# Performance work log

Hardware: AMD Instinct MI355X
Metric: run time of the kernel (lower is better)

## Reference

```python
import jax, jax.numpy as jnp
import numpy as np

B, N, E = 8, 4096, 65536
H, DH, GH = 4, 16, 64            # gat heads, head_dim, gat hidden
EDGE_EMBED = 16
D_FUSION = 640 + 64 + 640 + 40   # 1384


def setup_inputs() -> dict:
    key = jax.random.key(0)
    ks = jax.random.split(key, 24)
    rn = lambda i, shape, s=0.05: jax.random.normal(ks[i], shape, dtype=jnp.float32) * s
    return {
        'rnafm': rn(0, (B, 640), 1.0),
        'edit_delta': rn(1, (B, 640), 1.0),
        'hand_feat': rn(2, (B, 40), 1.0),
        'node_feats': rn(3, (B, N, 22), 1.0),
        'edge_index': jax.random.randint(ks[4], (B, 2, E), 0, N, dtype=jnp.int32),
        'edge_type': jax.random.randint(ks[5], (B, E), 0, 3, dtype=jnp.int32),
        'node_proj_w': rn(6, (GH, 22)), 'node_proj_b': jnp.zeros((GH,), jnp.float32),
        'gat_W': rn(7, (3, GH, GH)),
        'gat_a_src': rn(8, (3, H, DH)), 'gat_a_dst': rn(9, (3, H, DH)),
        'gat_a_edge': rn(10, (3, H, EDGE_EMBED)),
        'gat_edge_embed': rn(11, (3, 3, EDGE_EMBED)),
        'gat_ln_g': jnp.ones((3, GH), jnp.float32), 'gat_ln_b': jnp.zeros((3, GH), jnp.float32),
        'gat_out_w': rn(12, (64, GH)), 'gat_out_b': jnp.zeros((64,), jnp.float32),
        'enc1_w': rn(13, (256, D_FUSION)), 'enc1_b': jnp.zeros((256,), jnp.float32),
        'enc_ln_g': jnp.ones((256,), jnp.float32), 'enc_ln_b': jnp.zeros((256,), jnp.float32),
        'enc2_w': rn(14, (128, 256)), 'enc2_b': jnp.zeros((128,), jnp.float32),
        'bin_w': rn(15, (1, 128)), 'bin_b': jnp.zeros((1,), jnp.float32),
        'adp1_w': rn(16, (5, 32, 128)), 'adp1_b': jnp.zeros((5, 32), jnp.float32),
        'adp2_w': rn(17, (5, 1, 32)), 'adp2_b': jnp.zeros((5, 1), jnp.float32),
        'cls1_w': rn(18, (64, 128)), 'cls1_b': jnp.zeros((64,), jnp.float32),
        'cls2_w': rn(19, (6, 64)), 'cls2_b': jnp.zeros((6,), jnp.float32),
    }


def _layernorm(x, g, b, eps=1e-5):
    m = x.mean(-1, keepdims=True)
    v = ((x - m) ** 2).mean(-1, keepdims=True)
    return (x - m) / jnp.sqrt(v + eps) * g + b


def _gat_layer(x, src, dst, et, W, a_src, a_dst, a_edge, eemb, g, b):
    """x: [N, GH] -> [N, GH]; per-edge attention + scatter-softmax + scatter-add."""
    n = x.shape[0]
    h = x @ W.T                          # [N, GH]
    hh = h.reshape(n, H, DH)
    h_src, h_dst = hh[src], hh[dst]      # [E, H, DH] gathers
    attn = (jnp.einsum('ehd,hd->eh', h_src, a_src)
            + jnp.einsum('ehd,hd->eh', h_dst, a_dst)
            + eemb[et] @ a_edge.T)       # [E, H]
    attn = jnp.where(attn >= 0, attn, 0.2 * attn)  # leaky_relu(0.2)
    amax = jnp.maximum(jax.ops.segment_max(attn, dst, num_segments=n), -1e9)
    ex = jnp.exp(attn - amax[dst])
    denom = jax.ops.segment_sum(ex, dst, num_segments=n)
    an = ex / (denom[dst] + 1e-10)       # dropout is identity in eval
    agg = jax.ops.segment_sum(h_src * an[:, :, None], dst, num_segments=n)
    return _layernorm(agg.reshape(n, H * DH) + h, g, b)


def reference(rnafm, edit_delta, hand_feat, node_feats, edge_index, edge_type,
              node_proj_w, node_proj_b, gat_W, gat_a_src, gat_a_dst, gat_a_edge,
              gat_edge_embed, gat_ln_g, gat_ln_b, gat_out_w, gat_out_b,
              enc1_w, enc1_b, enc_ln_g, enc_ln_b, enc2_w, enc2_b,
              bin_w, bin_b, adp1_w, adp1_b, adp2_w, adp2_b,
              cls1_w, cls1_b, cls2_w, cls2_b):
    gelu = lambda t: jax.nn.gelu(t, approximate=False)

    def per_graph(nf, ei, et):
        x = nf @ node_proj_w.T + node_proj_b
        for l in range(3):
            x = gelu(_gat_layer(x, ei[0], ei[1], et, gat_W[l], gat_a_src[l],
                                gat_a_dst[l], gat_a_edge[l], gat_edge_embed[l],
                                gat_ln_g[l], gat_ln_b[l]))
        return x[x.shape[0] // 2]        # center node embedding

    gat_emb = jax.vmap(per_graph)(node_feats, edge_index, edge_type)   # [B, GH]
    gat_o = gat_emb @ gat_out_w.T + gat_out_b                          # [B, 64]
    fused = jnp.concatenate([rnafm, gat_o, edit_delta, hand_feat], axis=-1)
    h1 = _layernorm(gelu(fused @ enc1_w.T + enc1_b), enc_ln_g, enc_ln_b)
    shared = gelu(h1 @ enc2_w.T + enc2_b)                              # [B, 128]
    binary = (shared @ bin_w.T + bin_b)[:, 0]                          # [B]
    a1 = gelu(jnp.einsum('bf,hif->bhi', shared, adp1_w) + adp1_b)      # [B, 5, 32]
    per_enz = jnp.einsum('bhi,hi->bh', a1, adp2_w[:, 0, :]) + adp2_b[:, 0]  # [B, 5]
    cls = gelu(shared @ cls1_w.T + cls1_b) @ cls2_w.T + cls2_b         # [B, 6]
    return (binary, per_enz, cls, shared)
```

## Files before the change

### kernel.cpp

```cpp
#include <hip/hip_runtime.h>
#include <hip/hip_bf16.h>
#include <math.h>

#define BB 8
#define NN 4096
#define EE 65536
#define LOG2E 1.4426950408889634f

__device__ __forceinline__ float my_erf(float x){
  float ax = fabsf(x);
  float tt = 1.f/(1.f + 0.3275911f*ax);
  float poly = ((((1.061405429f*tt - 1.453152027f)*tt + 1.421413741f)*tt
                 - 0.284496736f)*tt + 0.254829592f)*tt;
  float y = 1.f - poly*expf(-ax*ax);
  return x >= 0.f ? y : -y;
}
__device__ __forceinline__ float gelu_f(float x){ return 0.5f*x*(1.0f + my_erf(x*0.7071067811865476f)); }
__device__ __forceinline__ float ld(const void* p, long i){ return ((const float*)p)[i]; }

__global__ __launch_bounds__(256) void k_pre(
    const void* __restrict__ nf, const void* __restrict__ pw, const void* __restrict__ pb,
    const void* __restrict__ W, const void* __restrict__ a_src, const void* __restrict__ a_dst,
    const void* __restrict__ a_edge, const void* __restrict__ eemb,
    const int* __restrict__ ei, const int* __restrict__ ety,
    float* __restrict__ h, float* __restrict__ sdot, float* __restrict__ ebt,
    int* __restrict__ cursor, int* __restrict__ csr, int b0, int nb, int NF){
  if ((int)blockIdx.x < NF){
    int fi = (int)blockIdx.x;
    int bpb = NF / nb;
    int b, q;
    if (nb == BB){ b = fi & 7; q = fi >> 3; }
    else         { b = fi / bpb; q = fi - b*bpb; }
    int e4 = q*256 + threadIdx.x;
    const int* base = ei + (long)(b0+b)*2*EE;
    int4 s4 = ((const int4*)base)[e4];
    int4 d4 = ((const int4*)(base + EE))[e4];
    int4 t4 = ((const int4*)(ety + (long)(b0+b)*EE))[e4];
    int* cb = cursor + b*NN;
    int ss[4] = {s4.x & (NN-1), s4.y & (NN-1), s4.z & (NN-1), s4.w & (NN-1)};
    int dd[4] = {d4.x & (NN-1), d4.y & (NN-1), d4.z & (NN-1), d4.w & (NN-1)};
    int tt[4] = {t4.x, t4.y, t4.z, t4.w};
    #pragma unroll
    for (int i=0;i<4;i++){
      int ty = tt[i]; ty = (ty < 0) ? 0 : (ty > 2 ? 2 : ty);
      int p = atomicAdd(&cb[dd[i]], 1);
      if (p < 64) csr[((long)(b*NN) + dd[i])*64 + p] = ss[i] | (ty << 12);
    }
    return;
  }

  __attribute__((aligned(16))) __shared__ float wlT[64*68];
  __attribute__((aligned(16))) __shared__ float nfl[32*24];
  __attribute__((aligned(16))) __shared__ float xs[32*68];
  int t = threadIdx.x;
  int lb = (int)blockIdx.x - NF;

  if (lb == 0 && t < 48){
    int ll = t >> 4, r = t & 15;
    if (r < 12){
      int ty = r >> 2, hd2 = r & 3;
      float s = 0.f;
      #pragma unroll
      for (int k=0;k<16;k++)
        s += ld(eemb, ll*48 + ty*16 + k) * ld(a_edge, ll*64 + hd2*16 + k);
      ebt[t] = s * LOG2E;
    }
  }
  {
    #pragma unroll
    for (int idx = t; idx < 1024; idx += 256){
      int row = idx >> 4, chunk = idx & 15;
      float4 wv = *((const float4*)((const float*)W + row*64 + chunk*4));
      *((float4*)&wlT[row*68 + chunk*4]) = wv;
    }
  }
  {
    long nfbase = ((long)b0*NN + (long)lb*32)*22;
    for (int idx = t; idx < 704; idx += 256){
      int row = idx / 22, k = idx - row*22;
      nfl[row*24 + k] = ld(nf, nfbase + idx);
    }
  }

  int w = t >> 6;
  int c = t & 63;
  int hd = c >> 4, dd = c & 15;
  long n0 = (long)lb*32 + w*8;

  float wreg[22];
  #pragma unroll
  for (int k = 0; k < 22; k++) wreg[k] = ld(pw, c*22 + k);
  float bias = ld(pb, c);
  __syncthreads();
  if (n0 >= nb*NN) return;

  #pragma unroll
  for (int i=0;i<8;i++){
    const float* nr = nfl + (w*8+i)*24;
    float a = bias;
    #pragma unroll
    for (int kc = 0; kc < 5; kc++){
      float4 nv = *((const float4*)&nr[kc*4]);
      a += nv.x*wreg[kc*4] + nv.y*wreg[kc*4+1] + nv.z*wreg[kc*4+2] + nv.w*wreg[kc*4+3];
    }
    a += nr[20]*wreg[20] + nr[21]*wreg[21];
    xs[(w*8+i)*68 + c] = a;
  }

  float acc[8] = {0.f,0.f,0.f,0.f,0.f,0.f,0.f,0.f};
  const float* xw = xs + (w*8)*68;
  const float* wr2 = wlT + c*68;
  #pragma unroll 4
  for (int kk=0;kk<16;kk++){
    float4 wv = *((const float4*)&wr2[kk*4]);
    #pragma unroll
    for (int i=0;i<8;i++){
      float4 xv = *((const float4*)&xw[i*68 + kk*4]);
      acc[i] += xv.x*wv.x + xv.y*wv.y + xv.z*wv.z + xv.w*wv.w;
    }
  }

  float cas = ld(a_src, c) * LOG2E;
  float cad = ld(a_dst, c) * LOG2E;
  #pragma unroll
  for (int i=0;i<8;i++){
    h[(n0+i)*64 + c] = acc[i];
    float ps = acc[i]*cas, pd = acc[i]*cad;
    #pragma unroll
    for (int o=8;o>=1;o>>=1){
      ps += __shfl_xor(ps,o,64);
      pd += __shfl_xor(pd,o,64);
    }
    if (dd == 0){
      sdot[(n0+i)*8 + hd]     = ps;
      sdot[(n0+i)*8 + 4 + hd] = pd;
    }
  }
}

__device__ __forceinline__ float gat_node(const float* __restrict__ hb,
    const float* __restrict__ sb, const int* __restrict__ cb, int dg,
    float sdP, float ebP0, float ebP1, float ebP2,
    float hdst, int c, int hd,
    const void* lng, const void* lnb, int l){
  int hL = c & 3;
  float denP = 0.f, acc = 0.f;
  int npass = (dg + 15) >> 4;
  for (int p = 0; p < npass; p++){
    int eidx = (p << 4) + (c >> 2);
    int pk = cb[eidx];
    int src = pk & 4095, ty = (pk >> 12) & 3;
    float av = sb[src*8 + hL] + sdP + (ty==0?ebP0:(ty==1?ebP1:ebP2));
    av = fmaxf(av, 0.2f*av);
    float ev = exp2f(av);
    if (eidx >= dg) ev = 0.f;
    denP += ev;
    int jmax = dg - (p << 4); if (jmax > 16) jmax = 16;
    #pragma unroll 4
    for (int j = 0; j < jmax; j++){
      float evj = __shfl(ev, j*4 + hd, 64);
      int sj = __builtin_amdgcn_readlane(pk, j*4) & 4095;
      acc += hb[(long)sj*64 + c] * evj;
    }
  }
  #pragma unroll
  for (int o=4;o<=32;o<<=1) denP += __shfl_xor(denP, o, 64);
  float den = __shfl(denP, hd, 64);
  float y = acc / (den + 1e-10f) + hdst;

  float s = y;
  #pragma unroll
  for (int o=32;o>=1;o>>=1) s += __shfl_xor(s, o, 64);
  float mean = s * (1.f/64.f);
  float d = y - mean;
  float vs = d*d;
  #pragma unroll
  for (int o=32;o>=1;o>>=1) vs += __shfl_xor(vs, o, 64);
  float var = vs * (1.f/64.f);
  float outv = d * rsqrtf(var + 1e-5f) * ld(lng, l*64+c) + ld(lnb, l*64+c);
  return gelu_f(outv);
}

__device__ __forceinline__ long swizzle_wave(int bi, int w, int nb){
  if (nb == BB) return (long)(bi & 7)*NN + (long)(bi >> 3)*4 + w;
  return (long)bi*4 + w;
}

__global__ __launch_bounds__(256) void k_gatlin(
    const float* __restrict__ hIn, const float* __restrict__ sdIn,
    const float* __restrict__ ebt,
    const int* __restrict__ cursor, const int* __restrict__ csr,
    const void* __restrict__ lng, const void* __restrict__ lnb,
    const void* __restrict__ W,
    const void* __restrict__ a_src, const void* __restrict__ a_dst,
    float* __restrict__ hOut, float* __restrict__ sdOut,
    int l, int nb){
  __attribute__((aligned(16))) __shared__ float wlT[64*68];
  __attribute__((aligned(16))) __shared__ float xs[4*68];
  int t = threadIdx.x;
  {
    #pragma unroll
    for (int idx = t; idx < 1024; idx += 256){
      int row = idx >> 4, chunk = idx & 15;
      float4 wv = *((const float4*)((const float*)W + (long)(l+1)*4096 + row*64 + chunk*4));
      *((float4*)&wlT[row*68 + chunk*4]) = wv;
    }
  }
  __syncthreads();

  int wloc = t >> 6;
  long wave = swizzle_wave(blockIdx.x, wloc, nb);
  if (wave >= nb*NN) return;
  int c  = t & 63;
  int hd = c >> 4, dd = c & 15, hL = c & 3;
  int b  = (int)(wave >> 12);

  float ebP0 = ebt[l*16 + 0 + hL];
  float ebP1 = ebt[l*16 + 4 + hL];
  float ebP2 = ebt[l*16 + 8 + hL];
  float sdP  = sdIn[wave*8 + 4 + hL];
  float hdst = hIn[wave*64 + c];
  int dg = __builtin_amdgcn_readfirstlane(cursor[wave]);
  dg = (dg < 0) ? 0 : (dg > 64 ? 64 : dg);
  const int* cb = csr + wave*64;
  const float* hb = hIn + (long)(b*NN)*64;
  const float* sb = sdIn + (long)(b*NN)*8;

  float g = gat_node(hb, sb, cb, dg, sdP, ebP0, ebP1, ebP2, hdst, c, hd, lng, lnb, l);

  xs[wloc*68 + c] = g;
  float ha = 0.f;
  const float* xw = xs + wloc*68;
  const float* wr = wlT + c*68;
  #pragma unroll 4
  for (int kk=0;kk<16;kk++){
    float4 xv = *((const float4*)&xw[kk*4]);
    float4 wv = *((const float4*)&wr[kk*4]);
    ha += xv.x*wv.x + xv.y*wv.y + xv.z*wv.z + xv.w*wv.w;
  }
  hOut[wave*64 + c] = ha;
  float cas = ld(a_src, (long)(l+1)*64 + c) * LOG2E;
  float cad = ld(a_dst, (long)(l+1)*64 + c) * LOG2E;
  float ps = ha*cas, pd = ha*cad;
  #pragma unroll
  for (int o=8;o>=1;o>>=1){
    ps += __shfl_xor(ps,o,64);
    pd += __shfl_xor(pd,o,64);
  }
  if (dd == 0){
    sdOut[wave*8 + hd]     = ps;
    sdOut[wave*8 + 4 + hd] = pd;
  }
}

__global__ __launch_bounds__(256) void k_gatlin2(
    const float* __restrict__ hIn, const float* __restrict__ sdIn,
    const float* __restrict__ ebt,
    const int* __restrict__ cursor, const int* __restrict__ csr,
    const void* __restrict__ lng, const void* __restrict__ lnb,
    const void* __restrict__ W,
    const void* __restrict__ a_src, const void* __restrict__ a_dst,
    float* __restrict__ hOut, float* __restrict__ sdOut,
    int l, int nb){
  __attribute__((aligned(16))) __shared__ float wlT[64*68];
  __attribute__((aligned(16))) __shared__ float xs[4*68];
  int t = threadIdx.x;
  {
    #pragma unroll
    for (int idx = t; idx < 1024; idx += 256){
      int row = idx >> 4, chunk = idx & 15;
      float4 wv = *((const float4*)((const float*)W + (long)(l+1)*4096 + row*64 + chunk*4));
      *((float4*)&wlT[row*68 + chunk*4]) = wv;
    }
  }
  __syncthreads();

  int wloc = t >> 6;
  int b  = (int)blockIdx.x % nb;
  int ib = (int)blockIdx.x / nb;
  int e  = ib*4 + wloc;
  long wcen = (long)b*NN + NN/2;
  int dgc = cursor[wcen];
  dgc = (dgc < 0) ? 0 : (dgc > 64 ? 64 : dgc);
  long wave;
  if (e == 0)            wave = wcen;
  else if (e <= dgc)     wave = (long)b*NN + (csr[wcen*64 + (e-1)] & 4095);
  else                   return;

  int c  = t & 63;
  int hd = c >> 4, dd = c & 15, hL = c & 3;

  float ebP0 = ebt[l*16 + 0 + hL];
  float ebP1 = ebt[l*16 + 4 + hL];
  float ebP2 = ebt[l*16 + 8 + hL];
  float sdP  = sdIn[wave*8 + 4 + hL];
  float hdst = hIn[wave*64 + c];
  int dg = __builtin_amdgcn_readfirstlane(cursor[wave]);
  dg = (dg < 0) ? 0 : (dg > 64 ? 64 : dg);
  const int* cb = csr + wave*64;
  const float* hb = hIn + (long)b*NN*64;
  const float* sb = sdIn + (long)b*NN*8;

  float g = gat_node(hb, sb, cb, dg, sdP, ebP0, ebP1, ebP2, hdst, c, hd, lng, lnb, l);

  xs[wloc*68 + c] = g;
  float ha = 0.f;
  const float* xw = xs + wloc*68;
  const float* wr = wlT + c*68;
  #pragma unroll 4
  for (int kk=0;kk<16;kk++){
    float4 xv = *((const float4*)&xw[kk*4]);
    float4 wv = *((const float4*)&wr[kk*4]);
    ha += xv.x*wv.x + xv.y*wv.y + xv.z*wv.z + xv.w*wv.w;
  }
  hOut[wave*64 + c] = ha;
  float cas = ld(a_src, (long)(l+1)*64 + c) * LOG2E;
  float cad = ld(a_dst, (long)(l+1)*64 + c) * LOG2E;
  float ps = ha*cas, pd = ha*cad;
  #pragma unroll
  for (int o=8;o>=1;o>>=1){
    ps += __shfl_xor(ps,o,64);
    pd += __shfl_xor(pd,o,64);
  }
  if (dd == 0){
    sdOut[wave*8 + hd]     = ps;
    sdOut[wave*8 + 4 + hd] = pd;
  }
}

__global__ __launch_bounds__(64) void k_gatfin(
    const float* __restrict__ hIn, const float* __restrict__ sdIn,
    const float* __restrict__ ebt,
    const int* __restrict__ cursor, const int* __restrict__ csr,
    const void* __restrict__ lng, const void* __restrict__ lnb,
    float* __restrict__ cemb, int l, int b0, int nb){
  int b = (int)blockIdx.x;
  if (b >= nb) return;
  long wave = (long)b*NN + NN/2;
  int c  = threadIdx.x & 63;
  int hd = c >> 4, hL = c & 3;

  float ebP0 = ebt[l*16 + 0 + hL];
  float ebP1 = ebt[l*16 + 4 + hL];
  float ebP2 = ebt[l*16 + 8 + hL];
  float sdP  = sdIn[wave*8 + 4 + hL];
  float hdst = hIn[wave*64 + c];
  int dg = __builtin_amdgcn_readfirstlane(cursor[wave]);
  dg = (dg < 0) ? 0 : (dg > 64 ? 64 : dg);
  const int* cb = csr + wave*64;
  const float* hb = hIn + (long)b*NN*64;
  const float* sb = sdIn + (long)b*NN*8;
  cemb[(b0+b)*64 + c] = gat_node(hb, sb, cb, dg, sdP, ebP0, ebP1, ebP2, hdst, c, hd, lng, lnb, l);
}

__global__ __launch_bounds__(256) void k_enc1(const float* __restrict__ ctr,
    const void* rnafm, const void* edelta, const void* hand,
    const void* gow, const void* gob,
    const void* e1w, const void* e1b, float* __restrict__ g1){
  __shared__ float fb[1384];
  __shared__ float femb[64];
  int b = blockIdx.x, t = threadIdx.x;
  for (int i=t;i<640;i+=256){
    fb[i]     = ld(rnafm,  b*640+i);
    fb[704+i] = ld(edelta, b*640+i);
  }
  if (t<40) fb[1344+t] = ld(hand, b*40+t);
  if (t>=64 && t<128){
    int cc = t-64;
    femb[cc] = ctr[b*64+cc];
  }
  __syncthreads();
  if (t<64){
    float acc = ld(gob, t);
    #pragma unroll 8
    for (int k=0;k<64;k++) acc += femb[k]*ld(gow, t*64+k);
    fb[640+t] = acc;
  }
  __syncthreads();
  int w = t >> 6, lane = t & 63;
  int c = blockIdx.y*4 + w;
  long wr = (long)c*1384;
  float acc = 0.f;
  #pragma unroll 7
  for (int i=0;i<21;i++){
    int k = lane + 64*i;
    acc += fb[k]*ld(e1w, wr+k);
  }
  if (lane < 40){
    int k = 1344+lane;
    acc += fb[k]*ld(e1w, wr+k);
  }
  #pragma unroll
  for (int o=32;o>=1;o>>=1) acc += __shfl_xor(acc, o, 64);
  if (lane==0) g1[b*256+c] = gelu_f(acc + ld(e1b, c));
}

__global__ __launch_bounds__(256) void k_enc2(const float* __restrict__ g1,
    const void* lng, const void* lnb, const void* e2w, const void* e2b,
    float* __restrict__ shs, float* __restrict__ out){
  __shared__ float red[256];
  __shared__ float h1s[256];
  int b = blockIdx.x, t = threadIdx.x;
  float g = g1[b*256+t];
  red[t] = g; __syncthreads();
  for (int s=128;s>=1;s>>=1){ if (t<s) red[t]+=red[t+s]; __syncthreads(); }
  float mean = red[0]*(1.f/256.f); __syncthreads();
  red[t] = (g-mean)*(g-mean); __syncthreads();
  for (int s=128;s>=1;s>>=1){ if (t<s) red[t]+=red[t+s]; __syncthreads(); }
  float var = red[0]*(1.f/256.f);
  h1s[t] = (g-mean)*rsqrtf(var+1e-5f)*ld(lng, t) + ld(lnb, t);
  __syncthreads();
  int w = t >> 6, lane = t & 63;
  int c = blockIdx.y*4 + w;
  long wr = (long)c*256;
  float acc = 0.f;
  #pragma unroll
  for (int i=0;i<4;i++){
    int k = lane + 64*i;
    acc += h1s[k]*ld(e2w, wr+k);
  }
  #pragma unroll
  for (int o=32;o>=1;o>>=1) acc += __shfl_xor(acc, o, 64);
  if (lane==0){
    float s = gelu_f(acc + ld(e2b, c));
    shs[b*128+c] = s;
    out[96 + b*128 + c] = s;
  }
}

__global__ __launch_bounds__(256) void k_mid(const float* __restrict__ shs,
    const void* a1w, const void* a1b, const void* c1w, const void* c1b,
    float* __restrict__ a1s, float* __restrict__ c1s){
  int b = blockIdx.x;
  int w = threadIdx.x >> 6, lane = threadIdx.x & 63;
  int idx = blockIdx.y*4 + w;
  const float* sb = shs + b*128;
  if (idx < 160){
    long wr = (long)idx*128;
    float acc = sb[lane]*ld(a1w, wr+lane) + sb[lane+64]*ld(a1w, wr+lane+64);
    #pragma unroll
    for (int o=32;o>=1;o>>=1) acc += __shfl_xor(acc, o, 64);
    if (lane==0) a1s[b*160+idx] = gelu_f(acc + ld(a1b, idx));
  } else {
    int c = idx - 160;
    long wr = (long)c*128;
    float acc = sb[lane]*ld(c1w, wr+lane) + sb[lane+64]*ld(c1w, wr+lane+64);
    #pragma unroll
    for (int o=32;o>=1;o>>=1) acc += __shfl_xor(acc, o, 64);
    if (lane==0) c1s[b*64+c] = gelu_f(acc + ld(c1b, c));
  }
}

__global__ __launch_bounds__(64) void k_fin(const float* __restrict__ shs,
    const float* __restrict__ a1s, const float* __restrict__ c1s,
    const void* binw, const void* binb, const void* a2w, const void* a2b,
    const void* c2w, const void* c2b,
    float* __restrict__ out){
  int b = blockIdx.x, t = threadIdx.x;
  {
    float p = shs[b*128+t]*ld(binw, t) + shs[b*128+t+64]*ld(binw, t+64);
    #pragma unroll
    for (int o=32;o>=1;o>>=1) p += __shfl_xor(p, o, 64);
    if (t==0) out[b] = p + ld(binb, 0);
  }
  if (t<5){
    float acc = ld(a2b, t);
    for (int i=0;i<32;i++) acc += a1s[b*160 + t*32+i]*ld(a2w, t*32+i);
    out[8 + b*5 + t] = acc;
  }
  if (t>=8 && t<14){
    int o = t-8;
    float acc = ld(c2b, o);
    for (int j=0;j<64;j++) acc += c1s[b*64+j]*ld(c2w, o*64+j);
    out[48 + b*6 + o] = acc;
  }
}

extern "C" void kernel_launch(void* const* d_in, const int* in_sizes, int n_in,
                              void* d_out, int out_size, void* d_ws, size_t ws_size,
                              hipStream_t stream) {
  const int* ei  = (const int*)d_in[4];
  const int* ety = (const int*)d_in[5];

  size_t need_full = 2048 + 512
                   + (size_t)4*((size_t)BB*NN)
                   + (size_t)4*((size_t)BB*NN*64)
                   + (size_t)4*3*((size_t)BB*NN*64)
                   + (size_t)4*2*((size_t)BB*NN*8)
                   + (size_t)4*(8*256 + 8*128 + 8*160 + 8*64 + 64);
  int nb = (ws_size >= need_full + (1u<<20)) ? BB : 1;

  char* ws = (char*)d_ws;
  float* cemb   = (float*)ws;
  float* ebt    = (float*)(ws + 2048 + 256);
  int*   cursor = (int*)(ws + 2048 + 512);
  int*   csr    = cursor + (size_t)nb*NN;
  float* hA     = (float*)(csr + (size_t)nb*NN*64);
  float* hB     = hA + (size_t)nb*NN*64;
  float* x      = hB + (size_t)nb*NN*64;
  float* sdotA  = x + (size_t)nb*NN*64;
  float* sdotB  = sdotA + (size_t)nb*NN*8;
  float* g1     = sdotB + (size_t)nb*NN*8;
  float* shs    = g1 + 8*256;
  float* a1s    = shs + 8*128;
  float* c1s    = a1s + 8*160;

  for (int b0 = 0; b0 < BB; b0 += nb){
    hipMemsetAsync(cursor, 0, (size_t)nb*NN*sizeof(int), stream);
    int NL = nb*NN/32;
    int NF = nb*(EE/1024);
    hipLaunchKernelGGL(k_pre, dim3(NF+NL), dim3(256), 0, stream,
                       d_in[3], d_in[6], d_in[7],
                       d_in[8], d_in[9], d_in[10], d_in[11], d_in[12],
                       ei, ety, hA, sdotA, ebt, cursor, csr, b0, nb, NF);
    hipLaunchKernelGGL(k_gatlin, dim3(nb*NN/4), dim3(256), 0, stream,
                       hA, sdotA, ebt, cursor, csr, d_in[13], d_in[14],
                       d_in[8], d_in[9], d_in[10], hB, sdotB, 0, nb);
    hipLaunchKernelGGL(k_gatlin2, dim3(nb*17), dim3(256), 0, stream,
                       hB, sdotB, ebt, cursor, csr, d_in[13], d_in[14],
                       d_in[8], d_in[9], d_in[10], hA, sdotA, 1, nb);
    hipLaunchKernelGGL(k_gatfin, dim3(nb), dim3(64), 0, stream,
                       hA, sdotA, ebt, cursor, csr, d_in[13], d_in[14],
                       cemb, 2, b0, nb);
  }

  hipLaunchKernelGGL(k_enc1, dim3(BB, 64), dim3(256), 0, stream,
                     cemb,
                     d_in[0], d_in[1], d_in[2], d_in[15], d_in[16],
                     d_in[17], d_in[18], g1);
  hipLaunchKernelGGL(k_enc2, dim3(BB, 32), dim3(256), 0, stream,
                     g1, d_in[19], d_in[20], d_in[21], d_in[22], shs, (float*)d_out);
  hipLaunchKernelGGL(k_mid,  dim3(BB, 56), dim3(256), 0, stream,
                     shs, d_in[25], d_in[26], d_in[29], d_in[30], a1s, c1s);
  hipLaunchKernelGGL(k_fin,  dim3(BB), dim3(64), 0, stream,
                     shs, a1s, c1s, d_in[23], d_in[24], d_in[27], d_in[28],
                     d_in[31], d_in[32], (float*)d_out);
}
```

Baseline: 236.3 us.

## Restrict first GAT layer to the 2-hop receptive cone of the center node

New measurement: 211.9 us. 1.12x faster.

```diff
diff --git a/kernel.cpp b/kernel.cpp
--- a/kernel.cpp
+++ b/kernel.cpp
@@ -181,12 +181,35 @@
   return gelu_f(outv);
 }
 
-__device__ __forceinline__ long swizzle_wave(int bi, int w, int nb){
-  if (nb == BB) return (long)(bi & 7)*NN + (long)(bi >> 3)*4 + w;
-  return (long)bi*4 + w;
-}
-
-__global__ __launch_bounds__(256) void k_gatlin(
+__device__ __forceinline__ void gat_linear_tail(float g, float* xs, const float* wlT,
+    const void* a_src, const void* a_dst, float* __restrict__ hOut,
+    float* __restrict__ sdOut, long wave, int wloc, int c, int hd, int dd, int l){
+  xs[wloc*68 + c] = g;
+  float ha = 0.f;
+  const float* xw = xs + wloc*68;
+  const float* wr = wlT + c*68;
+  #pragma unroll 4
+  for (int kk=0;kk<16;kk++){
+    float4 xv = *((const float4*)&xw[kk*4]);
+    float4 wv = *((const float4*)&wr[kk*4]);
+    ha += xv.x*wv.x + xv.y*wv.y + xv.z*wv.z + xv.w*wv.w;
+  }
+  hOut[wave*64 + c] = ha;
+  float cas = ld(a_src, (long)(l+1)*64 + c) * LOG2E;
+  float cad = ld(a_dst, (long)(l+1)*64 + c) * LOG2E;
+  float ps = ha*cas, pd = ha*cad;
+  #pragma unroll
+  for (int o=8;o>=1;o>>=1){
+    ps += __shfl_xor(ps,o,64);
+    pd += __shfl_xor(pd,o,64);
+  }
+  if (dd == 0){
+    sdOut[wave*8 + hd]     = ps;
+    sdOut[wave*8 + 4 + hd] = pd;
+  }
+}
+
+__global__ __launch_bounds__(256) void k_gatcone(
     const float* __restrict__ hIn, const float* __restrict__ sdIn,
     const float* __restrict__ ebt,
     const int* __restrict__ cursor, const int* __restrict__ csr,
@@ -198,6 +221,14 @@
   __attribute__((aligned(16))) __shared__ float wlT[64*68];
   __attribute__((aligned(16))) __shared__ float xs[4*68];
   int t = threadIdx.x;
+  int wloc = t >> 6;
+  int b  = (int)blockIdx.x % nb;
+  int ib = (int)blockIdx.x / nb;
+  long wcen = (long)b*NN + NN/2;
+  int dgc = cursor[wcen];
+  dgc = (dgc < 0) ? 0 : (dgc > 64 ? 64 : dgc);
+  int e0 = ib*4;
+  if (e0/65 > dgc) return;
   {
     #pragma unroll
     for (int idx = t; idx < 1024; idx += 256){
@@ -208,12 +239,20 @@
   }
   __syncthreads();
 
-  int wloc = t >> 6;
-  long wave = swizzle_wave(blockIdx.x, wloc, nb);
-  if (wave >= nb*NN) return;
+  int e = e0 + wloc;
+  int i = e / 65, j = e - i*65;
+  long wave = -1;
+  if (e < 4225 && i <= dgc){
+    long vi = (i == 0) ? wcen : (long)b*NN + (csr[wcen*64 + (i-1)] & 4095);
+    int dgi = cursor[vi];
+    dgi = (dgi < 0) ? 0 : (dgi > 64 ? 64 : dgi);
+    if (j == 0)            wave = vi;
+    else if (j <= dgi)     wave = (long)b*NN + (csr[vi*64 + (j-1)] & 4095);
+  }
+  if (wave < 0) return;
+
   int c  = t & 63;
   int hd = c >> 4, dd = c & 15, hL = c & 3;
-  int b  = (int)(wave >> 12);
 
   float ebP0 = ebt[l*16 + 0 + hL];
   float ebP1 = ebt[l*16 + 4 + hL];
@@ -223,34 +262,11 @@
   int dg = __builtin_amdgcn_readfirstlane(cursor[wave]);
   dg = (dg < 0) ? 0 : (dg > 64 ? 64 : dg);
   const int* cb = csr + wave*64;
-  const float* hb = hIn + (long)(b*NN)*64;
-  const float* sb = sdIn + (long)(b*NN)*8;
+  const float* hb = hIn + (long)b*NN*64;
+  const float* sb = sdIn + (long)b*NN*8;
 
   float g = gat_node(hb, sb, cb, dg, sdP, ebP0, ebP1, ebP2, hdst, c, hd, lng, lnb, l);
-
-  xs[wloc*68 + c] = g;
-  float ha = 0.f;
-  const float* xw = xs + wloc*68;
-  const float* wr = wlT + c*68;
-  #pragma unroll 4
-  for (int kk=0;kk<16;kk++){
-    float4 xv = *((const float4*)&xw[kk*4]);
-    float4 wv = *((const float4*)&wr[kk*4]);
-    ha += xv.x*wv.x + xv.y*wv.y + xv.z*wv.z + xv.w*wv.w;
-  }
-  hOut[wave*64 + c] = ha;
-  float cas = ld(a_src, (long)(l+1)*64 + c) * LOG2E;
-  float cad = ld(a_dst, (long)(l+1)*64 + c) * LOG2E;
-  float ps = ha*cas, pd = ha*cad;
-  #pragma unroll
-  for (int o=8;o>=1;o>>=1){
-    ps += __shfl_xor(ps,o,64);
-    pd += __shfl_xor(pd,o,64);
-  }
-  if (dd == 0){
-    sdOut[wave*8 + hd]     = ps;
-    sdOut[wave*8 + 4 + hd] = pd;
-  }
+  gat_linear_tail(g, xs, wlT, a_src, a_dst, hOut, sdOut, wave, wloc, c, hd, dd, l);
 }
 
 __global__ __launch_bounds__(256) void k_gatlin2(
@@ -302,30 +318,7 @@
   const float* sb = sdIn + (long)b*NN*8;
 
   float g = gat_node(hb, sb, cb, dg, sdP, ebP0, ebP1, ebP2, hdst, c, hd, lng, lnb, l);
-
-  xs[wloc*68 + c] = g;
-  float ha = 0.f;
-  const float* xw = xs + wloc*68;
-  const float* wr = wlT + c*68;
-  #pragma unroll 4
-  for (int kk=0;kk<16;kk++){
-    float4 xv = *((const float4*)&xw[kk*4]);
-    float4 wv = *((const float4*)&wr[kk*4]);
-    ha += xv.x*wv.x + xv.y*wv.y + xv.z*wv.z + xv.w*wv.w;
-  }
-  hOut[wave*64 + c] = ha;
-  float cas = ld(a_src, (long)(l+1)*64 + c) * LOG2E;
-  float cad = ld(a_dst, (long)(l+1)*64 + c) * LOG2E;
-  float ps = ha*cas, pd = ha*cad;
-  #pragma unroll
-  for (int o=8;o>=1;o>>=1){
-    ps += __shfl_xor(ps,o,64);
-    pd += __shfl_xor(pd,o,64);
-  }
-  if (dd == 0){
-    sdOut[wave*8 + hd]     = ps;
-    sdOut[wave*8 + 4 + hd] = pd;
-  }
+  gat_linear_tail(g, xs, wlT, a_src, a_dst, hOut, sdOut, wave, wloc, c, hd, dd, l);
 }
 
 __global__ __launch_bounds__(64) void k_gatfin(
@@ -513,7 +506,7 @@
                        d_in[3], d_in[6], d_in[7],
                        d_in[8], d_in[9], d_in[10], d_in[11], d_in[12],
                        ei, ety, hA, sdotA, ebt, cursor, csr, b0, nb, NF);
-    hipLaunchKernelGGL(k_gatlin, dim3(nb*NN/4), dim3(256), 0, stream,
+    hipLaunchKernelGGL(k_gatcone, dim3(nb*1057), dim3(256), 0, stream,
                        hA, sdotA, ebt, cursor, csr, d_in[13], d_in[14],
                        d_in[8], d_in[9], d_in[10], hB, sdotB, 0, nb);
     hipLaunchKernelGGL(k_gatlin2, dim3(nb*17), dim3(256), 0, stream,
```
